# Optimization experiments

Measured on AMD Instinct MI355X. Metric: run time of the kernel, lower is better.

## Reference

```python
import jax, jax.numpy as jnp
import numpy as np

NUM_NODES = 100000
DIM_E = 64
NEG_SLOPE = 0.01  # F.leaky_relu default


def setup_inputs() -> dict:
    key = jax.random.key(0)
    ks = jax.random.split(key, 8)
    edge_index = jax.random.randint(ks[0], (2, 1000000), 0, NUM_NODES, dtype=jnp.int64)
    # xavier_normal for id_embedding: std = sqrt(2/(fan_in+fan_out))
    std_emb = float(np.sqrt(2.0 / (NUM_NODES + DIM_E)))
    id_embedding = jax.random.normal(ks[1], (NUM_NODES, DIM_E), dtype=jnp.float32) * std_emb
    std_w = float(np.sqrt(2.0 / (DIM_E + DIM_E)))  # glorot for GCN lin weight [out, in]
    W1 = jax.random.normal(ks[2], (DIM_E, DIM_E), dtype=jnp.float32) * std_w
    W2 = jax.random.normal(ks[3], (DIM_E, DIM_E), dtype=jnp.float32) * std_w
    W3 = jax.random.normal(ks[4], (DIM_E, DIM_E), dtype=jnp.float32) * std_w
    b1 = jnp.zeros((DIM_E,), dtype=jnp.float32)
    b2 = jnp.zeros((DIM_E,), dtype=jnp.float32)
    b3 = jnp.zeros((DIM_E,), dtype=jnp.float32)
    return {"edge_index": edge_index, "id_embedding": id_embedding,
            "W1": W1, "b1": b1, "W2": W2, "b2": b2, "W3": W3, "b3": b3}


def _build_graph(edge_index, n):
    # symmetrize (as done in RealGCN.forward) then add self loops (PyG GCNConv default)
    ei = jnp.concatenate([edge_index, edge_index[::-1]], axis=1)
    loops = jnp.arange(n, dtype=ei.dtype)
    row = jnp.concatenate([ei[0], loops])  # source
    col = jnp.concatenate([ei[1], loops])  # destination
    deg = jax.ops.segment_sum(jnp.ones_like(col, dtype=jnp.float32), col, num_segments=n)
    dinv = jnp.where(deg > 0, jax.lax.rsqrt(deg), 0.0)
    norm = dinv[row] * dinv[col]  # [E_total]
    return row, col, norm


def _gcn_conv(x, row, col, norm, W, b, n):
    h = x @ W.T                                   # [N, D] linear transform
    msg = h[row] * norm[:, None]                  # gather + normalize
    out = jax.ops.segment_sum(msg, col, num_segments=n)  # scatter-add
    return out + b


def reference(edge_index, id_embedding, W1, b1, W2, b2, W3, b3):
    n = id_embedding.shape[0]
    row, col, norm = _build_graph(edge_index, n)
    # has_norm: L2-normalize rows (F.normalize, eps=1e-12)
    nrm = jnp.linalg.norm(id_embedding, axis=1, keepdims=True)
    x = id_embedding / jnp.maximum(nrm, 1e-12)
    x1 = jax.nn.leaky_relu(_gcn_conv(x, row, col, norm, W1, b1, n), NEG_SLOPE)
    x2 = jax.nn.leaky_relu(_gcn_conv(x1, row, col, norm, W2, b2, n), NEG_SLOPE)
    x3 = _gcn_conv(x1, row, col, norm, W3, b3, n)  # note: layer 3 has no activation
    return x + x1 + x2 + x3
```

## Files before the change

### kernel.cpp

```cpp
#include <hip/hip_runtime.h>
#include <math.h>

#define DIM 64
#define NEG_SLOPE 0.01f

typedef unsigned short bfraw;
typedef unsigned int uint32;

__device__ __forceinline__ bfraw f2bf(float f) {
    unsigned int u = __float_as_uint(f);
    unsigned int r = (u + 0x7FFFu + ((u >> 16) & 1u)) >> 16;
    return (bfraw)r;
}
__device__ __forceinline__ float bflo(uint32 u) { return __uint_as_float(u << 16); }
__device__ __forceinline__ float bfhi(uint32 u) { return __uint_as_float(u & 0xFFFF0000u); }

__global__ void k_initcur(int* __restrict__ bcur, int nbuckets, int capS) {
    int b = blockIdx.x * blockDim.x + threadIdx.x;
    if (b < nbuckets) bcur[b * 16] = b * capS;
}

#define EPW 4096

__global__ __launch_bounds__(256) void k_bin(const int* __restrict__ ei, int E,
                                             uint32* __restrict__ stage,
                                             int* __restrict__ bcur, int shift, int sbits) {
    __shared__ int hist[256];
    __shared__ int cur[256];
    int t = threadIdx.x;
    hist[t] = 0;
    __syncthreads();
    int e0 = blockIdx.x * EPW;
    int e1 = e0 + EPW < E ? e0 + EPW : E;
    uint32 lmask = (1u << shift) - 1u;
    for (int e = e0 + t; e < e1; e += 256) {
        int u = ei[e], v = ei[E + e];
        atomicAdd(&hist[u >> shift], 1);
        atomicAdd(&hist[v >> shift], 1);
    }
    __syncthreads();
    cur[t] = hist[t] > 0 ? atomicAdd(&bcur[t * 16], hist[t]) : 0;
    __syncthreads();
    for (int e = e0 + t; e < e1; e += 256) {
        int u = ei[e], v = ei[E + e];
        int s1 = atomicAdd(&cur[v >> shift], 1);
        stage[s1] = (((uint32)v & lmask) << sbits) | (uint32)u;
        int s2 = atomicAdd(&cur[u >> shift], 1);
        stage[s2] = (((uint32)u & lmask) << sbits) | (uint32)v;
    }
}

__global__ __launch_bounds__(256) void k_bucket(const uint32* __restrict__ stage,
                                                const int* __restrict__ bcur,
                                                int* __restrict__ offsets,
                                                int* __restrict__ oend,
                                                int* __restrict__ adj,
                                                float* __restrict__ dinv,
                                                int n, int shift, int sbits,
                                                int capS, int capA) {
    __shared__ int deg[2048];
    __shared__ int scan[256];
    int t = threadIdx.x;
    int span  = 1 << shift;
    int node0 = blockIdx.x << shift;
    int cnt = n - node0 < span ? n - node0 : span;
    uint32 smask = (1u << sbits) - 1u;
    for (int i = t; i < cnt; i += 256) deg[i] = 0;
    __syncthreads();
    int jbeg = blockIdx.x * capS;
    int jend = bcur[blockIdx.x * 16];
    for (int j = jbeg + t; j < jend; j += 256)
        atomicAdd(&deg[stage[j] >> sbits], 1);
    __syncthreads();
    int per  = span >> 8;
    int base = t * per;
    int s = 0;
    for (int k = 0; k < per; k++) { int i = base + k; if (i < cnt) s += deg[i] + 1; }
    scan[t] = s;
    __syncthreads();
    for (int off = 1; off < 256; off <<= 1) {
        int v = (t >= off) ? scan[t - off] : 0;
        __syncthreads();
        scan[t] += v;
        __syncthreads();
    }
    int run = blockIdx.x * capA + scan[t] - s;
    for (int k = 0; k < per; k++) {
        int i = base + k;
        if (i < cnt) {
            int d = deg[i];
            offsets[node0 + i] = run;
            oend[node0 + i]    = run + 1 + d;
            dinv[node0 + i] = rsqrtf(1.0f + (float)d);
            adj[run] = node0 + i;
            deg[i] = run + 1;
            run += d + 1;
        }
    }
    __syncthreads();
    for (int j = jbeg + t; j < jend; j += 256) {
        uint32 r = stage[j];
        int slot = atomicAdd(&deg[r >> sbits], 1);
        adj[slot] = (int)(r & smask);
    }
}

__global__ void k_normalize(const float* __restrict__ x, const float* __restrict__ dinv,
                            float* __restrict__ xn, bfraw* __restrict__ xnw, int n) {
    int row  = (blockIdx.x * blockDim.x + threadIdx.x) >> 6;
    int lane = threadIdx.x & 63;
    if (row >= n) return;
    float v = x[row * DIM + lane];
    float s = v * v;
    #pragma unroll
    for (int off = 32; off; off >>= 1) s += __shfl_xor(s, off);
    float scale = 1.0f / fmaxf(sqrtf(s), 1e-12f);
    float xv = v * scale;
    xn[row * DIM + lane] = xv;
    xnw[row * DIM + lane] = f2bf(xv * dinv[row]);
}

#define ACC8(p) { a0 += bflo(p.x); a1 += bfhi(p.x); a2 += bflo(p.y); a3 += bfhi(p.y); \
                  a4 += bflo(p.z); a5 += bfhi(p.z); a6 += bflo(p.w); a7 += bfhi(p.w); }

__global__ void k_gather(const int* __restrict__ adj, const int* __restrict__ offsets,
                         const int* __restrict__ oend,
                         const float* __restrict__ dinv,
                         const bfraw* __restrict__ srcw,
                         float* __restrict__ dst, int n) {
    int w    = (blockIdx.x * blockDim.x + threadIdx.x) >> 6;
    int lane = threadIdx.x & 63;
    if (w >= n) return;
    int oct = lane >> 3;
    int ol  = lane & 7;
    int beg = offsets[w], end = oend[w];
    float dd = dinv[w];
    const uint4* rows = (const uint4*)srcw;
    float a0 = 0.f, a1 = 0.f, a2 = 0.f, a3 = 0.f;
    float a4 = 0.f, a5 = 0.f, a6 = 0.f, a7 = 0.f;
    int j = beg;
    for (; j + 32 <= end; j += 32) {
        int s0 = adj[j + oct];
        int s1 = adj[j + 8 + oct];
        int s2 = adj[j + 16 + oct];
        int s3 = adj[j + 24 + oct];
        uint4 p0 = rows[(size_t)s0 * 8 + ol];
        uint4 p1 = rows[(size_t)s1 * 8 + ol];
        uint4 p2 = rows[(size_t)s2 * 8 + ol];
        uint4 p3 = rows[(size_t)s3 * 8 + ol];
        ACC8(p0) ACC8(p1) ACC8(p2) ACC8(p3)
    }
    if (j + 16 <= end) {
        int s0 = adj[j + oct];
        int s1 = adj[j + 8 + oct];
        uint4 p0 = rows[(size_t)s0 * 8 + ol];
        uint4 p1 = rows[(size_t)s1 * 8 + ol];
        ACC8(p0) ACC8(p1)
        j += 16;
    }
    if (j + 8 <= end) {
        int s0 = adj[j + oct];
        uint4 p0 = rows[(size_t)s0 * 8 + ol];
        ACC8(p0)
        j += 8;
    }
    int rem = end - j;
    if (oct < rem) {
        int s0 = adj[j + oct];
        uint4 p0 = rows[(size_t)s0 * 8 + ol];
        ACC8(p0)
    }
    a0 += __shfl_xor(a0, 8); a0 += __shfl_xor(a0, 16); a0 += __shfl_xor(a0, 32);
    a1 += __shfl_xor(a1, 8); a1 += __shfl_xor(a1, 16); a1 += __shfl_xor(a1, 32);
    a2 += __shfl_xor(a2, 8); a2 += __shfl_xor(a2, 16); a2 += __shfl_xor(a2, 32);
    a3 += __shfl_xor(a3, 8); a3 += __shfl_xor(a3, 16); a3 += __shfl_xor(a3, 32);
    a4 += __shfl_xor(a4, 8); a4 += __shfl_xor(a4, 16); a4 += __shfl_xor(a4, 32);
    a5 += __shfl_xor(a5, 8); a5 += __shfl_xor(a5, 16); a5 += __shfl_xor(a5, 32);
    a6 += __shfl_xor(a6, 8); a6 += __shfl_xor(a6, 16); a6 += __shfl_xor(a6, 32);
    a7 += __shfl_xor(a7, 8); a7 += __shfl_xor(a7, 16); a7 += __shfl_xor(a7, 32);
    if (lane < 8) {
        float4 o1, o2;
        o1.x = dd * a0; o1.y = dd * a1; o1.z = dd * a2; o1.w = dd * a3;
        o2.x = dd * a4; o2.y = dd * a5; o2.z = dd * a6; o2.w = dd * a7;
        float4* outp = (float4*)(dst + (size_t)w * DIM);
        outp[2 * ol]     = o1;
        outp[2 * ol + 1] = o2;
    }
}

__global__ __launch_bounds__(256) void k_linear_rt(
    const float* __restrict__ in, const float* __restrict__ W,
    const float* __restrict__ b, const float* __restrict__ dinv,
    float* __restrict__ out, bfraw* __restrict__ outw, int n)
{
    __shared__ float  sIn[64][65];
    __shared__ uint32 sWp[64][32];
    int tid = threadIdx.x;
    int r0  = blockIdx.x * 64;
    #pragma unroll
    for (int i = 0; i < 8; i++) {
        int idx = tid + i * 256;
        int k = idx & 63, cp = idx >> 6;
        sWp[k][cp] = (uint32)f2bf(W[(2 * cp) * DIM + k]) |
                     ((uint32)f2bf(W[(2 * cp + 1) * DIM + k]) << 16);
    }
    int lim = (n - r0 < 64 ? n - r0 : 64) * DIM;
    for (int idx = tid; idx < lim; idx += 256)
        sIn[idx >> 6][idx & 63] = in[(size_t)r0 * DIM + idx];
    __syncthreads();

    int ri = (tid >> 4) << 2;
    int ci = (tid & 15) << 2;
    int cp = ci >> 1;
    float acc[4][4];
    #pragma unroll
    for (int j = 0; j < 4; j++) {
        float bj = b[ci + j];
        #pragma unroll
        for (int i = 0; i < 4; i++) acc[i][j] = bj;
    }
    #pragma unroll 2
    for (int k4 = 0; k4 < 16; k4++) {
        int k = k4 * 4;
        float4 A0 = *(const float4*)&sIn[ri + 0][k];
        float4 A1 = *(const float4*)&sIn[ri + 1][k];
        float4 A2 = *(const float4*)&sIn[ri + 2][k];
        float4 A3 = *(const float4*)&sIn[ri + 3][k];
        #pragma unroll
        for (int kk = 0; kk < 4; kk++) {
            uint2 uw = *(const uint2*)&sWp[k + kk][cp];
            float w0 = bflo(uw.x), w1 = bfhi(uw.x);
            float w2 = bflo(uw.y), w3 = bfhi(uw.y);
            float a0 = kk == 0 ? A0.x : kk == 1 ? A0.y : kk == 2 ? A0.z : A0.w;
            float a1 = kk == 0 ? A1.x : kk == 1 ? A1.y : kk == 2 ? A1.z : A1.w;
            float a2 = kk == 0 ? A2.x : kk == 1 ? A2.y : kk == 2 ? A2.z : A2.w;
            float a3 = kk == 0 ? A3.x : kk == 1 ? A3.y : kk == 2 ? A3.z : A3.w;
            acc[0][0] = fmaf(a0, w0, acc[0][0]); acc[0][1] = fmaf(a0, w1, acc[0][1]);
            acc[0][2] = fmaf(a0, w2, acc[0][2]); acc[0][3] = fmaf(a0, w3, acc[0][3]);
            acc[1][0] = fmaf(a1, w0, acc[1][0]); acc[1][1] = fmaf(a1, w1, acc[1][1]);
            acc[1][2] = fmaf(a1, w2, acc[1][2]); acc[1][3] = fmaf(a1, w3, acc[1][3]);
            acc[2][0] = fmaf(a2, w0, acc[2][0]); acc[2][1] = fmaf(a2, w1, acc[2][1]);
            acc[2][2] = fmaf(a2, w2, acc[2][2]); acc[2][3] = fmaf(a2, w3, acc[2][3]);
            acc[3][0] = fmaf(a3, w0, acc[3][0]); acc[3][1] = fmaf(a3, w1, acc[3][1]);
            acc[3][2] = fmaf(a3, w2, acc[3][2]); acc[3][3] = fmaf(a3, w3, acc[3][3]);
        }
    }
    #pragma unroll
    for (int i = 0; i < 4; i++) {
        int r = r0 + ri + i;
        if (r >= n) break;
        float dd = dinv[r];
        float4 o;
        o.x = acc[i][0] > 0.f ? acc[i][0] : NEG_SLOPE * acc[i][0];
        o.y = acc[i][1] > 0.f ? acc[i][1] : NEG_SLOPE * acc[i][1];
        o.z = acc[i][2] > 0.f ? acc[i][2] : NEG_SLOPE * acc[i][2];
        o.w = acc[i][3] > 0.f ? acc[i][3] : NEG_SLOPE * acc[i][3];
        *(float4*)&out[(size_t)r * DIM + ci] = o;
        ushort4 ow;
        ow.x = f2bf(o.x * dd); ow.y = f2bf(o.y * dd);
        ow.z = f2bf(o.z * dd); ow.w = f2bf(o.w * dd);
        *(ushort4*)&outw[(size_t)r * DIM + ci] = ow;
    }
}

__global__ __launch_bounds__(256) void k_final_rt(
    const float* __restrict__ agg, const float* __restrict__ xn,
    const float* __restrict__ x1,
    const float* __restrict__ W2, const float* __restrict__ b2,
    const float* __restrict__ W3, const float* __restrict__ b3,
    float* __restrict__ out, int n)
{
    __shared__ float  sIn[64][65];
    __shared__ uint32 sW2p[64][32];
    __shared__ uint32 sW3p[64][32];
    int tid = threadIdx.x;
    int r0  = blockIdx.x * 64;
    #pragma unroll
    for (int i = 0; i < 8; i++) {
        int idx = tid + i * 256;
        int k = idx & 63, cp = idx >> 6;
        sW2p[k][cp] = (uint32)f2bf(W2[(2 * cp) * DIM + k]) |
                      ((uint32)f2bf(W2[(2 * cp + 1) * DIM + k]) << 16);
        sW3p[k][cp] = (uint32)f2bf(W3[(2 * cp) * DIM + k]) |
                      ((uint32)f2bf(W3[(2 * cp + 1) * DIM + k]) << 16);
    }
    int lim = (n - r0 < 64 ? n - r0 : 64) * DIM;
    for (int idx = tid; idx < lim; idx += 256)
        sIn[idx >> 6][idx & 63] = agg[(size_t)r0 * DIM + idx];
    __syncthreads();

    int ri = (tid >> 4) << 2;
    int ci = (tid & 15) << 2;
    int cp = ci >> 1;
    float acc2[4][4], acc3[4][4];
    #pragma unroll
    for (int j = 0; j < 4; j++) {
        float bj2 = b2[ci + j], bj3 = b3[ci + j];
        #pragma unroll
        for (int i = 0; i < 4; i++) { acc2[i][j] = bj2; acc3[i][j] = bj3; }
    }
    #pragma unroll 2
    for (int k4 = 0; k4 < 16; k4++) {
        int k = k4 * 4;
        float4 A0 = *(const float4*)&sIn[ri + 0][k];
        float4 A1 = *(const float4*)&sIn[ri + 1][k];
        float4 A2 = *(const float4*)&sIn[ri + 2][k];
        float4 A3 = *(const float4*)&sIn[ri + 3][k];
        #pragma unroll
        for (int kk = 0; kk < 4; kk++) {
            uint2 u2 = *(const uint2*)&sW2p[k + kk][cp];
            uint2 u3 = *(const uint2*)&sW3p[k + kk][cp];
            float a0 = kk == 0 ? A0.x : kk == 1 ? A0.y : kk == 2 ? A0.z : A0.w;
            float a1 = kk == 0 ? A1.x : kk == 1 ? A1.y : kk == 2 ? A1.z : A1.w;
            float a2 = kk == 0 ? A2.x : kk == 1 ? A2.y : kk == 2 ? A2.z : A2.w;
            float a3 = kk == 0 ? A3.x : kk == 1 ? A3.y : kk == 2 ? A3.z : A3.w;
            float u0 = bflo(u2.x), u1 = bfhi(u2.x), u2c = bflo(u2.y), u3c = bfhi(u2.y);
            float v0 = bflo(u3.x), v1 = bfhi(u3.x), v2c = bflo(u3.y), v3c = bfhi(u3.y);
            acc2[0][0] = fmaf(a0, u0, acc2[0][0]); acc2[0][1] = fmaf(a0, u1, acc2[0][1]);
            acc2[0][2] = fmaf(a0, u2c, acc2[0][2]); acc2[0][3] = fmaf(a0, u3c, acc2[0][3]);
            acc2[1][0] = fmaf(a1, u0, acc2[1][0]); acc2[1][1] = fmaf(a1, u1, acc2[1][1]);
            acc2[1][2] = fmaf(a1, u2c, acc2[1][2]); acc2[1][3] = fmaf(a1, u3c, acc2[1][3]);
            acc2[2][0] = fmaf(a2, u0, acc2[2][0]); acc2[2][1] = fmaf(a2, u1, acc2[2][1]);
            acc2[2][2] = fmaf(a2, u2c, acc2[2][2]); acc2[2][3] = fmaf(a2, u3c, acc2[2][3]);
            acc2[3][0] = fmaf(a3, u0, acc2[3][0]); acc2[3][1] = fmaf(a3, u1, acc2[3][1]);
            acc2[3][2] = fmaf(a3, u2c, acc2[3][2]); acc2[3][3] = fmaf(a3, u3c, acc2[3][3]);
            acc3[0][0] = fmaf(a0, v0, acc3[0][0]); acc3[0][1] = fmaf(a0, v1, acc3[0][1]);
            acc3[0][2] = fmaf(a0, v2c, acc3[0][2]); acc3[0][3] = fmaf(a0, v3c, acc3[0][3]);
            acc3[1][0] = fmaf(a1, v0, acc3[1][0]); acc3[1][1] = fmaf(a1, v1, acc3[1][1]);
            acc3[1][2] = fmaf(a1, v2c, acc3[1][2]); acc3[1][3] = fmaf(a1, v3c, acc3[1][3]);
            acc3[2][0] = fmaf(a2, v0, acc3[2][0]); acc3[2][1] = fmaf(a2, v1, acc3[2][1]);
            acc3[2][2] = fmaf(a2, v2c, acc3[2][2]); acc3[2][3] = fmaf(a2, v3c, acc3[2][3]);
            acc3[3][0] = fmaf(a3, v0, acc3[3][0]); acc3[3][1] = fmaf(a3, v1, acc3[3][1]);
            acc3[3][2] = fmaf(a3, v2c, acc3[3][2]); acc3[3][3] = fmaf(a3, v3c, acc3[3][3]);
        }
    }
    #pragma unroll
    for (int i = 0; i < 4; i++) {
        int r = r0 + ri + i;
        if (r >= n) break;
        size_t base = (size_t)r * DIM + ci;
        float4 vxn = *(const float4*)&xn[base];
        float4 vx1 = *(const float4*)&x1[base];
        float4 o;
        float e0 = acc2[i][0] > 0.f ? acc2[i][0] : NEG_SLOPE * acc2[i][0];
        float e1 = acc2[i][1] > 0.f ? acc2[i][1] : NEG_SLOPE * acc2[i][1];
        float e2 = acc2[i][2] > 0.f ? acc2[i][2] : NEG_SLOPE * acc2[i][2];
        float e3 = acc2[i][3] > 0.f ? acc2[i][3] : NEG_SLOPE * acc2[i][3];
        o.x = vxn.x + vx1.x + e0 + acc3[i][0];
        o.y = vxn.y + vx1.y + e1 + acc3[i][1];
        o.z = vxn.z + vx1.z + e2 + acc3[i][2];
        o.w = vxn.w + vx1.w + e3 + acc3[i][3];
        *(float4*)&out[base] = o;
    }
}


extern "C" void kernel_launch(void* const* d_in, const int* in_sizes, int n_in,
                              void* d_out, int out_size, void* d_ws, size_t ws_size,
                              hipStream_t stream) {
    const int*   ei  = (const int*)d_in[0];
    const float* emb = (const float*)d_in[1];
    const float* W1  = (const float*)d_in[2];
    const float* b1  = (const float*)d_in[3];
    const float* W2  = (const float*)d_in[4];
    const float* b2  = (const float*)d_in[5];
    const float* W3  = (const float*)d_in[6];
    const float* b3  = (const float*)d_in[7];
    float* out = (float*)d_out;

    int E = in_sizes[0] / 2;
    int n = in_sizes[1] / DIM;
    size_t nD = (size_t)n * DIM;

    int shift = 9;
    while ((((size_t)n + ((size_t)1 << shift) - 1) >> shift) > 256) shift++;
    int nbuckets = (int)(((size_t)n + ((size_t)1 << shift) - 1) >> shift);
    int sbits = 32 - shift;
    int span  = 1 << shift;

    int capS = (int)(2 * (size_t)E / nbuckets + (2 * (size_t)E) / (4 * (size_t)nbuckets) + 2048);
    if ((size_t)nbuckets * capS > nD) capS = (int)(nD / nbuckets);
    int capA = capS + span;

    size_t np   = ((size_t)n + 1023) & ~1023ull;
    size_t adjn = ((size_t)nbuckets * capA + 31) & ~31ull;
    int*   bcur    = (int*)d_ws;
    int*   offsets = bcur + 4096;
    int*   oendA   = offsets + np;
    float* dinv    = (float*)(oendA + np);
    float* xn      = dinv + np;
    float* x1      = xn + nD;
    float* agg     = x1 + nD;
    int*   adj     = (int*)(agg + nD);
    bfraw* xnw     = (bfraw*)(adj + adjn);
    bfraw* x1w     = xnw + nD;
    uint32* stage  = (uint32*)agg;

    const int B = 256;

    k_initcur<<<1, B, 0, stream>>>(bcur, nbuckets, capS);
    k_bin    <<<(E + EPW - 1) / EPW, B, 0, stream>>>(ei, E, stage, bcur, shift, sbits);
    k_bucket <<<nbuckets, B, 0, stream>>>(stage, bcur, offsets, oendA, adj, dinv,
                                          n, shift, sbits, capS, capA);

    k_normalize<<<(n + 3) / 4, B, 0, stream>>>(emb, dinv, xn, xnw, n);

    k_gather   <<<(n + 3) / 4, B, 0, stream>>>(adj, offsets, oendA, dinv, xnw, agg, n);
    k_linear_rt<<<(n + 63) / 64, B, 0, stream>>>(agg, W1, b1, dinv, x1, x1w, n);

    k_gather   <<<(n + 3) / 4, B, 0, stream>>>(adj, offsets, oendA, dinv, x1w, agg, n);
    k_final_rt <<<(n + 63) / 64, B, 0, stream>>>(agg, xn, x1, W2, b2, W3, b3, out, n);
}
```

Baseline: 219.4 us.

## Store intermediate activations and aggregates in bf16, replace init kernel with memset

After: 219.2 us, median of 2. No clear change (-0.1%).

```diff
diff --git a/kernel.cpp b/kernel.cpp
--- a/kernel.cpp
+++ b/kernel.cpp
@@ -14,17 +14,16 @@
 }
 __device__ __forceinline__ float bflo(uint32 u) { return __uint_as_float(u << 16); }
 __device__ __forceinline__ float bfhi(uint32 u) { return __uint_as_float(u & 0xFFFF0000u); }
-
-__global__ void k_initcur(int* __restrict__ bcur, int nbuckets, int capS) {
-    int b = blockIdx.x * blockDim.x + threadIdx.x;
-    if (b < nbuckets) bcur[b * 16] = b * capS;
+__device__ __forceinline__ uint32 pack2(float lo, float hi) {
+    return (uint32)f2bf(lo) | ((uint32)f2bf(hi) << 16);
 }
 
 #define EPW 4096
 
 __global__ __launch_bounds__(256) void k_bin(const int* __restrict__ ei, int E,
                                              uint32* __restrict__ stage,
-                                             int* __restrict__ bcur, int shift, int sbits) {
+                                             int* __restrict__ bcur, int shift, int sbits,
+                                             int capS) {
     __shared__ int hist[256];
     __shared__ int cur[256];
     int t = threadIdx.x;
@@ -39,7 +38,7 @@
         atomicAdd(&hist[v >> shift], 1);
     }
     __syncthreads();
-    cur[t] = hist[t] > 0 ? atomicAdd(&bcur[t * 16], hist[t]) : 0;
+    cur[t] = hist[t] > 0 ? (t * capS + atomicAdd(&bcur[t * 16], hist[t])) : 0;
     __syncthreads();
     for (int e = e0 + t; e < e1; e += 256) {
         int u = ei[e], v = ei[E + e];
@@ -68,7 +67,7 @@
     for (int i = t; i < cnt; i += 256) deg[i] = 0;
     __syncthreads();
     int jbeg = blockIdx.x * capS;
-    int jend = bcur[blockIdx.x * 16];
+    int jend = jbeg + bcur[blockIdx.x * 16];
     for (int j = jbeg + t; j < jend; j += 256)
         atomicAdd(&deg[stage[j] >> sbits], 1);
     __syncthreads();
@@ -106,7 +105,7 @@
 }
 
 __global__ void k_normalize(const float* __restrict__ x, const float* __restrict__ dinv,
-                            float* __restrict__ xn, bfraw* __restrict__ xnw, int n) {
+                            bfraw* __restrict__ xnb, bfraw* __restrict__ xnw, int n) {
     int row  = (blockIdx.x * blockDim.x + threadIdx.x) >> 6;
     int lane = threadIdx.x & 63;
     if (row >= n) return;
@@ -116,7 +115,7 @@
     for (int off = 32; off; off >>= 1) s += __shfl_xor(s, off);
     float scale = 1.0f / fmaxf(sqrtf(s), 1e-12f);
     float xv = v * scale;
-    xn[row * DIM + lane] = xv;
+    xnb[row * DIM + lane] = f2bf(xv);
     xnw[row * DIM + lane] = f2bf(xv * dinv[row]);
 }
 
@@ -127,7 +126,7 @@
                          const int* __restrict__ oend,
                          const float* __restrict__ dinv,
                          const bfraw* __restrict__ srcw,
-                         float* __restrict__ dst, int n) {
+                         bfraw* __restrict__ dstb, int n) {
     int w    = (blockIdx.x * blockDim.x + threadIdx.x) >> 6;
     int lane = threadIdx.x & 63;
     if (w >= n) return;
@@ -179,19 +178,20 @@
     a6 += __shfl_xor(a6, 8); a6 += __shfl_xor(a6, 16); a6 += __shfl_xor(a6, 32);
     a7 += __shfl_xor(a7, 8); a7 += __shfl_xor(a7, 16); a7 += __shfl_xor(a7, 32);
     if (lane < 8) {
-        float4 o1, o2;
-        o1.x = dd * a0; o1.y = dd * a1; o1.z = dd * a2; o1.w = dd * a3;
-        o2.x = dd * a4; o2.y = dd * a5; o2.z = dd * a6; o2.w = dd * a7;
-        float4* outp = (float4*)(dst + (size_t)w * DIM);
-        outp[2 * ol]     = o1;
-        outp[2 * ol + 1] = o2;
-    }
-}
+        uint4 o;
+        o.x = pack2(dd * a0, dd * a1);
+        o.y = pack2(dd * a2, dd * a3);
+        o.z = pack2(dd * a4, dd * a5);
+        o.w = pack2(dd * a6, dd * a7);
+        ((uint4*)(dstb + (size_t)w * DIM))[ol] = o;
+    }
+}
+
 
 __global__ __launch_bounds__(256) void k_linear_rt(
-    const float* __restrict__ in, const float* __restrict__ W,
+    const bfraw* __restrict__ inb, const float* __restrict__ W,
     const float* __restrict__ b, const float* __restrict__ dinv,
-    float* __restrict__ out, bfraw* __restrict__ outw, int n)
+    bfraw* __restrict__ outb, bfraw* __restrict__ outw, int n)
 {
     __shared__ float  sIn[64][65];
     __shared__ uint32 sWp[64][32];
@@ -204,9 +204,13 @@
         sWp[k][cp] = (uint32)f2bf(W[(2 * cp) * DIM + k]) |
                      ((uint32)f2bf(W[(2 * cp + 1) * DIM + k]) << 16);
     }
-    int lim = (n - r0 < 64 ? n - r0 : 64) * DIM;
-    for (int idx = tid; idx < lim; idx += 256)
-        sIn[idx >> 6][idx & 63] = in[(size_t)r0 * DIM + idx];
+    int limu = ((n - r0 < 64 ? n - r0 : 64) * DIM) >> 1;
+    const uint32* inu = (const uint32*)(inb + (size_t)r0 * DIM);
+    for (int idx = tid; idx < limu; idx += 256) {
+        uint32 u = inu[idx];
+        int r = idx >> 5, c = (idx & 31) * 2;
+        sIn[r][c] = bflo(u); sIn[r][c + 1] = bfhi(u);
+    }
     __syncthreads();
 
     int ri = (tid >> 4) << 2;
@@ -250,22 +254,23 @@
         int r = r0 + ri + i;
         if (r >= n) break;
         float dd = dinv[r];
-        float4 o;
-        o.x = acc[i][0] > 0.f ? acc[i][0] : NEG_SLOPE * acc[i][0];
-        o.y = acc[i][1] > 0.f ? acc[i][1] : NEG_SLOPE * acc[i][1];
-        o.z = acc[i][2] > 0.f ? acc[i][2] : NEG_SLOPE * acc[i][2];
-        o.w = acc[i][3] > 0.f ? acc[i][3] : NEG_SLOPE * acc[i][3];
-        *(float4*)&out[(size_t)r * DIM + ci] = o;
+        float e0 = acc[i][0] > 0.f ? acc[i][0] : NEG_SLOPE * acc[i][0];
+        float e1 = acc[i][1] > 0.f ? acc[i][1] : NEG_SLOPE * acc[i][1];
+        float e2 = acc[i][2] > 0.f ? acc[i][2] : NEG_SLOPE * acc[i][2];
+        float e3 = acc[i][3] > 0.f ? acc[i][3] : NEG_SLOPE * acc[i][3];
+        ushort4 ob;
+        ob.x = f2bf(e0); ob.y = f2bf(e1); ob.z = f2bf(e2); ob.w = f2bf(e3);
+        *(ushort4*)&outb[(size_t)r * DIM + ci] = ob;
         ushort4 ow;
-        ow.x = f2bf(o.x * dd); ow.y = f2bf(o.y * dd);
-        ow.z = f2bf(o.z * dd); ow.w = f2bf(o.w * dd);
+        ow.x = f2bf(e0 * dd); ow.y = f2bf(e1 * dd);
+        ow.z = f2bf(e2 * dd); ow.w = f2bf(e3 * dd);
         *(ushort4*)&outw[(size_t)r * DIM + ci] = ow;
     }
 }
 
 __global__ __launch_bounds__(256) void k_final_rt(
-    const float* __restrict__ agg, const float* __restrict__ xn,
-    const float* __restrict__ x1,
+    const bfraw* __restrict__ aggb, const bfraw* __restrict__ xnb,
+    const bfraw* __restrict__ x1b,
     const float* __restrict__ W2, const float* __restrict__ b2,
     const float* __restrict__ W3, const float* __restrict__ b3,
     float* __restrict__ out, int n)
@@ -284,9 +289,13 @@
         sW3p[k][cp] = (uint32)f2bf(W3[(2 * cp) * DIM + k]) |
                       ((uint32)f2bf(W3[(2 * cp + 1) * DIM + k]) << 16);
     }
-    int lim = (n - r0 < 64 ? n - r0 : 64) * DIM;
-    for (int idx = tid; idx < lim; idx += 256)
-        sIn[idx >> 6][idx & 63] = agg[(size_t)r0 * DIM + idx];
+    int limu = ((n - r0 < 64 ? n - r0 : 64) * DIM) >> 1;
+    const uint32* inu = (const uint32*)(aggb + (size_t)r0 * DIM);
+    for (int idx = tid; idx < limu; idx += 256) {
+        uint32 u = inu[idx];
+        int r = idx >> 5, c = (idx & 31) * 2;
+        sIn[r][c] = bflo(u); sIn[r][c + 1] = bfhi(u);
+    }
     __syncthreads();
 
     int ri = (tid >> 4) << 2;
@@ -339,17 +348,17 @@
         int r = r0 + ri + i;
         if (r >= n) break;
         size_t base = (size_t)r * DIM + ci;
-        float4 vxn = *(const float4*)&xn[base];
-        float4 vx1 = *(const float4*)&x1[base];
+        uint2 uxn = *(const uint2*)&xnb[base];
+        uint2 ux1 = *(const uint2*)&x1b[base];
         float4 o;
         float e0 = acc2[i][0] > 0.f ? acc2[i][0] : NEG_SLOPE * acc2[i][0];
         float e1 = acc2[i][1] > 0.f ? acc2[i][1] : NEG_SLOPE * acc2[i][1];
         float e2 = acc2[i][2] > 0.f ? acc2[i][2] : NEG_SLOPE * acc2[i][2];
         float e3 = acc2[i][3] > 0.f ? acc2[i][3] : NEG_SLOPE * acc2[i][3];
-        o.x = vxn.x + vx1.x + e0 + acc3[i][0];
-        o.y = vxn.y + vx1.y + e1 + acc3[i][1];
-        o.z = vxn.z + vx1.z + e2 + acc3[i][2];
-        o.w = vxn.w + vx1.w + e3 + acc3[i][3];
+        o.x = bflo(uxn.x) + bflo(ux1.x) + e0 + acc3[i][0];
+        o.y = bfhi(uxn.x) + bfhi(ux1.x) + e1 + acc3[i][1];
+        o.z = bflo(uxn.y) + bflo(ux1.y) + e2 + acc3[i][2];
+        o.w = bfhi(uxn.y) + bfhi(ux1.y) + e3 + acc3[i][3];
         *(float4*)&out[base] = o;
     }
 }
@@ -379,7 +388,7 @@
     int span  = 1 << shift;
 
     int capS = (int)(2 * (size_t)E / nbuckets + (2 * (size_t)E) / (4 * (size_t)nbuckets) + 2048);
-    if ((size_t)nbuckets * capS > nD) capS = (int)(nD / nbuckets);
+    if ((size_t)nbuckets * capS > nD / 2) capS = (int)((nD / 2) / nbuckets);
     int capA = capS + span;
 
     size_t np   = ((size_t)n + 1023) & ~1023ull;
@@ -388,26 +397,26 @@
     int*   offsets = bcur + 4096;
     int*   oendA   = offsets + np;
     float* dinv    = (float*)(oendA + np);
-    float* xn      = dinv + np;
-    float* x1      = xn + nD;
-    float* agg     = x1 + nD;
-    int*   adj     = (int*)(agg + nD);
+    bfraw* aggb    = (bfraw*)(dinv + np);
+    int*   adj     = (int*)(aggb + nD);
     bfraw* xnw     = (bfraw*)(adj + adjn);
     bfraw* x1w     = xnw + nD;
-    uint32* stage  = (uint32*)agg;
+    bfraw* xnb     = x1w + nD;
+    bfraw* x1b     = xnb + nD;
+    uint32* stage  = (uint32*)aggb;
 
     const int B = 256;
 
-    k_initcur<<<1, B, 0, stream>>>(bcur, nbuckets, capS);
-    k_bin    <<<(E + EPW - 1) / EPW, B, 0, stream>>>(ei, E, stage, bcur, shift, sbits);
-    k_bucket <<<nbuckets, B, 0, stream>>>(stage, bcur, offsets, oendA, adj, dinv,
-                                          n, shift, sbits, capS, capA);
-
-    k_normalize<<<(n + 3) / 4, B, 0, stream>>>(emb, dinv, xn, xnw, n);
-
-    k_gather   <<<(n + 3) / 4, B, 0, stream>>>(adj, offsets, oendA, dinv, xnw, agg, n);
-    k_linear_rt<<<(n + 63) / 64, B, 0, stream>>>(agg, W1, b1, dinv, x1, x1w, n);
-
-    k_gather   <<<(n + 3) / 4, B, 0, stream>>>(adj, offsets, oendA, dinv, x1w, agg, n);
-    k_final_rt <<<(n + 63) / 64, B, 0, stream>>>(agg, xn, x1, W2, b2, W3, b3, out, n);
-}
+    hipMemsetAsync(bcur, 0, 4096 * sizeof(int), stream);
+    k_bin   <<<(E + EPW - 1) / EPW, B, 0, stream>>>(ei, E, stage, bcur, shift, sbits, capS);
+    k_bucket<<<nbuckets, B, 0, stream>>>(stage, bcur, offsets, oendA, adj, dinv,
+                                         n, shift, sbits, capS, capA);
+
+    k_normalize<<<(n + 3) / 4, B, 0, stream>>>(emb, dinv, xnb, xnw, n);
+
+    k_gather   <<<(n + 3) / 4, B, 0, stream>>>(adj, offsets, oendA, dinv, xnw, aggb, n);
+    k_linear_rt<<<(n + 63) / 64, B, 0, stream>>>(aggb, W1, b1, dinv, x1b, x1w, n);
+
+    k_gather   <<<(n + 3) / 4, B, 0, stream>>>(adj, offsets, oendA, dinv, x1w, aggb, n);
+    k_final_rt <<<(n + 63) / 64, B, 0, stream>>>(aggb, xnb, x1b, W2, b2, W3, b3, out, n);
+}
```
